# Optimization experiments

Hardware: AMD Instinct MI355X
Metric: run time of the kernel (lower is better)

The kernel has to match this reference:

```python
import jax, jax.numpy as jnp
import numpy as np


def setup_inputs() -> dict:
    key = jax.random.key(0)
    ks = jax.random.split(key, 7)
    B, S, D, H, Dh = 4, 2048, 1024, 16, 64
    return {
        "query_input": jax.random.normal(ks[0], (B, S, D), jnp.float32),
        "key_input": jax.random.normal(ks[1], (B, S, D), jnp.float32),
        "value_input": jax.random.normal(ks[2], (B, S, D), jnp.float32),
        "Wq": jax.random.normal(ks[3], (D, H, Dh), jnp.float32) * 0.03,
        "Wk": jax.random.normal(ks[4], (D, H, Dh), jnp.float32) * 0.03,
        "Wv": jax.random.normal(ks[5], (D, H, Dh), jnp.float32) * 0.03,
        "Wo": jax.random.normal(ks[6], (H, Dh, D), jnp.float32) * 0.03,
    }


def reference(query_input, key_input, value_input, Wq, Wk, Wv, Wo):
    # Projections: [B,S,D] x [D,H,Dh] -> [B,S,H,Dh]
    q = jnp.einsum("bsd,dhk->bshk", query_input, Wq)
    k = jnp.einsum("bsd,dhk->bshk", key_input, Wk)
    v = jnp.einsum("bsd,dhk->bshk", value_input, Wv)
    depth = Wq.shape[-1]
    q = q * (depth ** -0.5)
    # logits: [B,H,F,T]  (F = query len, T = key len)
    logits = jnp.einsum("bthk,bfhk->bhft", k, q)
    weights = jax.nn.softmax(logits, axis=-1)
    # attention output: [B,F,H,Dh]
    ctx = jnp.einsum("bhft,bthk->bfhk", weights, v)
    # output projection: [B,F,H,Dh] x [H,Dh,D] -> [B,F,D]
    return jnp.einsum("bfhk,hkd->bfd", ctx, Wo)
```

## Files before the change

kernel.cpp:

```cpp
#include <hip/hip_runtime.h>
#include <stdint.h>

typedef __bf16 bf16;
typedef __bf16 bf16x4 __attribute__((ext_vector_type(4)));
typedef __bf16 bf16x8 __attribute__((ext_vector_type(8)));
typedef float f32x4 __attribute__((ext_vector_type(4)));

#define AS1 __attribute__((address_space(1)))
#define AS3 __attribute__((address_space(3)))

__device__ __forceinline__ void async16(void* lds, const void* g) {
    __builtin_amdgcn_global_load_lds((AS1 void*)g, (AS3 void*)lds, 16, 0, 0);
}

__global__ __launch_bounds__(256) void prep(
    const float* __restrict__ x0, const float* __restrict__ x1,
    const float* __restrict__ x2,
    bf16* __restrict__ y0, bf16* __restrict__ y1, bf16* __restrict__ y2,
    const float* __restrict__ s0, const float* __restrict__ s1,
    const float* __restrict__ s2, const float* __restrict__ s3,
    bf16* __restrict__ d0, bf16* __restrict__ d1,
    bf16* __restrict__ d2, bf16* __restrict__ d3) {
    const int z = blockIdx.z;
    const int t = threadIdx.x;
    if (z < 3) {
        const float* x = z == 0 ? x0 : z == 1 ? x1 : x2;
        bf16* y = z == 0 ? y0 : z == 1 ? y1 : y2;
        int i = (blockIdx.x * 256 + t) * 8;
        f32x4 a = *(const f32x4*)(x + i);
        f32x4 b = *(const f32x4*)(x + i + 4);
        bf16x8 o;
#pragma unroll
        for (int j = 0; j < 4; ++j) { o[j] = (bf16)a[j]; o[4 + j] = (bf16)b[j]; }
        *(bf16x8*)(y + i) = o;
        return;
    }
    const int bx = blockIdx.x;
    if (bx >= 1024) return;
    const int wsel = bx >> 8, tile = bx & 255;
    const float* W = wsel == 0 ? s0 : wsel == 1 ? s1 : wsel == 2 ? s2 : s3;
    bf16* Wt = wsel == 0 ? d0 : wsel == 1 ? d1 : wsel == 2 ? d2 : d3;
    const int k0 = (tile >> 4) * 64, n0 = (tile & 15) * 64;
    __shared__ float Ts[64 * 65];
    const int c = t & 63, r0 = t >> 6;
#pragma unroll
    for (int i = 0; i < 16; ++i) {
        int r = r0 + i * 4;
        Ts[r * 65 + c] = W[(size_t)(k0 + r) * 1024 + n0 + c];
    }
    __syncthreads();
#pragma unroll
    for (int i = 0; i < 16; ++i) {
        int r = r0 + i * 4;
        Wt[(size_t)(n0 + r) * 1024 + k0 + c] = (bf16)Ts[c * 65 + r];
    }
}

template <typename OutT>
__device__ __forceinline__ void gemm_body(const bf16* __restrict__ A,
                                          const bf16* __restrict__ Bt,
                                          OutT* __restrict__ C,
                                          int N, int K, float scale,
                                          int m0, int n0,
                                          bf16* As, bf16* Bs) {
    const int t = threadIdx.x;
    const int lane = t & 63;
    const int w = t >> 6;
    const int l15 = lane & 15;
    const int quad = lane >> 4;
    const int wm = w >> 1, wn = w & 1;

    f32x4 acc[4][4];
#pragma unroll
    for (int i = 0; i < 4; ++i)
#pragma unroll
        for (int j = 0; j < 4; ++j) acc[i][j] = (f32x4){0.f, 0.f, 0.f, 0.f};

    const bf16* gA[4];
    const bf16* gB[4];
#pragma unroll
    for (int j = 0; j < 4; ++j) {
        int c = j * 256 + t;
        int row = c >> 3, g = (c & 7) ^ (row & 7);
        gA[j] = A + (size_t)(m0 + row) * K + g * 8;
        gB[j] = Bt + (size_t)(n0 + row) * K + g * 8;
    }

    for (int k0 = 0; k0 < K; k0 += 64) {
        __syncthreads();
#pragma unroll
        for (int j = 0; j < 4; ++j) {
            async16(As + (j * 256 + w * 64) * 8, gA[j] + k0);
            async16(Bs + (j * 256 + w * 64) * 8, gB[j] + k0);
        }
        __syncthreads();
#pragma unroll
        for (int kk = 0; kk < 2; ++kk) {
            bf16x8 af[4], bfv[4];
#pragma unroll
            for (int mi = 0; mi < 4; ++mi) {
                int r = wm * 64 + mi * 16 + l15;
                af[mi] = *(const bf16x8*)&As[r * 64 + (((kk * 4 + quad) ^ (r & 7)) * 8)];
            }
#pragma unroll
            for (int ni = 0; ni < 4; ++ni) {
                int r = wn * 64 + ni * 16 + l15;
                bfv[ni] = *(const bf16x8*)&Bs[r * 64 + (((kk * 4 + quad) ^ (r & 7)) * 8)];
            }
#pragma unroll
            for (int mi = 0; mi < 4; ++mi)
#pragma unroll
                for (int ni = 0; ni < 4; ++ni)
                    acc[mi][ni] = __builtin_amdgcn_mfma_f32_16x16x32_bf16(
                        af[mi], bfv[ni], acc[mi][ni], 0, 0, 0);
        }
    }

#pragma unroll
    for (int mi = 0; mi < 4; ++mi)
#pragma unroll
        for (int ni = 0; ni < 4; ++ni)
#pragma unroll
            for (int r = 0; r < 4; ++r) {
                int row = m0 + wm * 64 + mi * 16 + quad * 4 + r;
                int col = n0 + wn * 64 + ni * 16 + l15;
                C[(size_t)row * N + col] = (OutT)(acc[mi][ni][r] * scale);
            }
}

__global__ __launch_bounds__(256) void gemm_qkv(
    const bf16* __restrict__ Xq, const bf16* __restrict__ Xk, const bf16* __restrict__ Xv,
    const bf16* __restrict__ Wqt, const bf16* __restrict__ Wkt, const bf16* __restrict__ Wvt,
    bf16* __restrict__ Qb, bf16* __restrict__ Kb, bf16* __restrict__ VtG) {
    __shared__ __align__(16) bf16 As[128 * 64];
    __shared__ __align__(16) bf16 Bs[128 * 64];
    const int z = blockIdx.z;
    const int blk = blockIdx.x;
    const bf16* A; const bf16* Bt; bf16* C; int N; float scale; int m0, n0;
    if (z == 0) { A = Xq; Bt = Wqt; C = Qb; N = 1024; scale = 0.125f;
                  m0 = (blk >> 3) * 128; n0 = (blk & 7) * 128; }
    else if (z == 1) { A = Xk; Bt = Wkt; C = Kb; N = 1024; scale = 1.0f;
                  m0 = (blk >> 3) * 128; n0 = (blk & 7) * 128; }
    else { A = Wvt; Bt = Xv; C = VtG; N = 8192; scale = 1.0f;
                  m0 = (blk >> 6) * 128; n0 = (blk & 63) * 128; }
    gemm_body<bf16>(A, Bt, C, N, 1024, scale, m0, n0, As, Bs);
}

__global__ __launch_bounds__(256) void gemm_out(const bf16* __restrict__ A,
                                                const bf16* __restrict__ Bt,
                                                float* __restrict__ C) {
    __shared__ __align__(16) bf16 As[128 * 64];
    __shared__ __align__(16) bf16 Bs[128 * 64];
    gemm_body<float>(A, Bt, C, 1024, 1024, 1.0f, blockIdx.y * 128, blockIdx.x * 128,
                     As, Bs);
}

__global__ __launch_bounds__(256) void attn_fa(const bf16* __restrict__ Q,
                                               const bf16* __restrict__ K,
                                               const bf16* __restrict__ Vt,
                                               bf16* __restrict__ O) {
    __shared__ __align__(16) bf16 Ks[2][64 * 64];
    __shared__ __align__(16) bf16 Vs[2][64 * 64];
    __shared__ __align__(16) bf16 Pt[4][32 * 72];

    const int t = threadIdx.x;
    const int lane = t & 63;
    const int w = t >> 6;
    const int l15 = lane & 15;
    const int quad = lane >> 4;
    const int bh = blockIdx.y;
    const int b = bh >> 4, h = bh & 15;
    const int q0 = blockIdx.x * 128;
    const size_t baseQ = (size_t)b * 2048 * 1024 + (size_t)h * 64;
    const float L2E = 1.44269504088896340736f;

    const int r0s = t >> 3,          g0s = (t & 7) ^ (r0s & 7);
    const int r1s = (t + 256) >> 3,  g1s = ((t + 256) & 7) ^ (r1s & 7);
    const bf16* gK0 = K + baseQ + (size_t)r0s * 1024 + g0s * 8;
    const bf16* gK1 = K + baseQ + (size_t)r1s * 1024 + g1s * 8;
    const bf16* gV0 = Vt + (size_t)(h * 64 + r0s) * 8192 + (size_t)b * 2048 + g0s * 8;
    const bf16* gV1 = Vt + (size_t)(h * 64 + r1s) * 8192 + (size_t)b * 2048 + g1s * 8;

    bf16x8 qf[2][2];
#pragma unroll
    for (int mi = 0; mi < 2; ++mi)
#pragma unroll
        for (int kk = 0; kk < 2; ++kk)
            qf[mi][kk] = *(const bf16x8*)(Q + baseQ +
                (size_t)(q0 + w * 32 + mi * 16 + l15) * 1024 + kk * 32 + quad * 8);

    f32x4 accO[4][2];
    float l_part[2] = {0.f, 0.f};
#pragma unroll
    for (int nd = 0; nd < 4; ++nd)
#pragma unroll
        for (int mi = 0; mi < 2; ++mi) accO[nd][mi] = (f32x4){0.f, 0.f, 0.f, 0.f};

    auto swz = [&](int r, int g) { return (r * 8 + (g ^ (r & 7))) * 8; };
    auto stage = [&](int t0, int bi) {
        async16((bf16*)Ks[bi] + w * 512,        gK0 + (size_t)t0 * 1024);
        async16((bf16*)Ks[bi] + 2048 + w * 512, gK1 + (size_t)t0 * 1024);
        async16((bf16*)Vs[bi] + w * 512,        gV0 + t0);
        async16((bf16*)Vs[bi] + 2048 + w * 512, gV1 + t0);
    };

    stage(0, 0);

    for (int it = 0; it < 32; ++it) {
        __syncthreads();
        if (it + 1 < 32) stage((it + 1) * 64, (it + 1) & 1);
        const bf16* Kb = Ks[it & 1];
        const bf16* Vb = Vs[it & 1];

        f32x4 accS[4][2];
#pragma unroll
        for (int nt = 0; nt < 4; ++nt)
#pragma unroll
            for (int mi = 0; mi < 2; ++mi) accS[nt][mi] = (f32x4){0.f, 0.f, 0.f, 0.f};
#pragma unroll
        for (int kk = 0; kk < 2; ++kk) {
            bf16x8 kf[4];
#pragma unroll
            for (int nt = 0; nt < 4; ++nt)
                kf[nt] = *(const bf16x8*)&Kb[swz(nt * 16 + l15, kk * 4 + quad)];
#pragma unroll
            for (int nt = 0; nt < 4; ++nt)
#pragma unroll
                for (int mi = 0; mi < 2; ++mi)
                    accS[nt][mi] = __builtin_amdgcn_mfma_f32_16x16x32_bf16(
                        kf[nt], qf[mi][kk], accS[nt][mi], 0, 0, 0);
        }

        bf16* Pp = &Pt[w][0];
#pragma unroll
        for (int mi = 0; mi < 2; ++mi) {
            float rs = 0.f;
#pragma unroll
            for (int nt = 0; nt < 4; ++nt) {
                bf16x4 pk;
#pragma unroll
                for (int r = 0; r < 4; ++r) {
                    float p = __builtin_amdgcn_exp2f(accS[nt][mi][r] * L2E);
                    rs += p;
                    pk[r] = (bf16)p;
                }
                *(bf16x4*)&Pp[(mi * 16 + l15) * 72 + nt * 16 + quad * 4] = pk;
            }
            l_part[mi] += rs;
        }

#pragma unroll
        for (int kk = 0; kk < 2; ++kk) {
            bf16x8 vf[4], pf[2];
#pragma unroll
            for (int nd = 0; nd < 4; ++nd)
                vf[nd] = *(const bf16x8*)&Vb[swz(nd * 16 + l15, kk * 4 + quad)];
#pragma unroll
            for (int mi = 0; mi < 2; ++mi)
                pf[mi] = *(const bf16x8*)&Pp[(mi * 16 + l15) * 72 + kk * 32 + quad * 8];
#pragma unroll
            for (int nd = 0; nd < 4; ++nd)
#pragma unroll
                for (int mi = 0; mi < 2; ++mi)
                    accO[nd][mi] = __builtin_amdgcn_mfma_f32_16x16x32_bf16(
                        vf[nd], pf[mi], accO[nd][mi], 0, 0, 0);
        }
    }

    float inv[2];
#pragma unroll
    for (int mi = 0; mi < 2; ++mi) {
        float l = l_part[mi];
        l += __shfl_xor(l, 16);
        l += __shfl_xor(l, 32);
        inv[mi] = 1.0f / l;
    }

#pragma unroll
    for (int mi = 0; mi < 2; ++mi) {
        size_t rowoff = baseQ + (size_t)(q0 + w * 32 + mi * 16 + l15) * 1024;
#pragma unroll
        for (int nd = 0; nd < 4; ++nd) {
            bf16x4 o;
#pragma unroll
            for (int r = 0; r < 4; ++r) o[r] = (bf16)(accO[nd][mi][r] * inv[mi]);
            *(bf16x4*)&O[rowoff + nd * 16 + quad * 4] = o;
        }
    }
}

extern "C" void kernel_launch(void* const* d_in, const int* in_sizes, int n_in,
                              void* d_out, int out_size, void* d_ws, size_t ws_size,
                              hipStream_t stream) {
    const float* qin = (const float*)d_in[0];
    const float* kin = (const float*)d_in[1];
    const float* vin = (const float*)d_in[2];
    const float* Wq = (const float*)d_in[3];
    const float* Wk = (const float*)d_in[4];
    const float* Wv = (const float*)d_in[5];
    const float* Wo = (const float*)d_in[6];
    float* out = (float*)d_out;

    char* ws = (char*)d_ws;
    bf16* Xq  = (bf16*)(ws);
    bf16* Xk  = (bf16*)(ws + ((size_t)16 << 20));
    bf16* Xv  = (bf16*)(ws + ((size_t)32 << 20));
    bf16* Qb  = (bf16*)(ws + ((size_t)48 << 20));
    bf16* Kb  = (bf16*)(ws + ((size_t)64 << 20));
    bf16* VtG = (bf16*)(ws + ((size_t)80 << 20));
    bf16* Cb  = (bf16*)(ws);
    bf16* Wqt = (bf16*)(ws + ((size_t)96 << 20));
    bf16* Wkt = Wqt + 1024 * 1024;
    bf16* Wvt = Wkt + 1024 * 1024;
    bf16* Wot = Wvt + 1024 * 1024;

    prep<<<dim3(4096, 1, 4), 256, 0, stream>>>(qin, kin, vin, Xq, Xk, Xv,
                                               Wq, Wk, Wv, Wo, Wqt, Wkt, Wvt, Wot);
    gemm_qkv<<<dim3(512, 1, 3), 256, 0, stream>>>(Xq, Xk, Xv, Wqt, Wkt, Wvt,
                                                  Qb, Kb, VtG);
    attn_fa<<<dim3(16, 64), 256, 0, stream>>>(Qb, Kb, VtG, Cb);
    gemm_out<<<dim3(8, 64), 256, 0, stream>>>(Cb, Wot, out);
}
```

Before: 341.8 us.

## Fold log2e into Q scale, single-buffer K/V, vectorize row-sum accumulation

Folds the log2(e) factor into the Q projection scale so the attention kernel no longer multiplies every logit before exp2. It drops the double-buffered K/V staging in favour of a single buffer, loaded synchronously with a barrier before and after each tile, which halves K/V LDS use and may allow more resident blocks. Row sums now accumulate as 4-wide vectors and are reduced once at the end. The cost is losing the overlap of global loads with compute, so each iteration waits for its K/V tile to arrive.

```diff
diff --git a/kernel.cpp b/kernel.cpp
--- a/kernel.cpp
+++ b/kernel.cpp
@@ -137,7 +137,8 @@
     const int z = blockIdx.z;
     const int blk = blockIdx.x;
     const bf16* A; const bf16* Bt; bf16* C; int N; float scale; int m0, n0;
-    if (z == 0) { A = Xq; Bt = Wqt; C = Qb; N = 1024; scale = 0.125f;
+    if (z == 0) { A = Xq; Bt = Wqt; C = Qb; N = 1024;
+                  scale = 0.125f * 1.44269504088896340736f;
                   m0 = (blk >> 3) * 128; n0 = (blk & 7) * 128; }
     else if (z == 1) { A = Xk; Bt = Wkt; C = Kb; N = 1024; scale = 1.0f;
                   m0 = (blk >> 3) * 128; n0 = (blk & 7) * 128; }
@@ -159,8 +160,8 @@
                                                const bf16* __restrict__ K,
                                                const bf16* __restrict__ Vt,
                                                bf16* __restrict__ O) {
-    __shared__ __align__(16) bf16 Ks[2][64 * 64];
-    __shared__ __align__(16) bf16 Vs[2][64 * 64];
+    __shared__ __align__(16) bf16 Ks[64 * 64];
+    __shared__ __align__(16) bf16 Vs[64 * 64];
     __shared__ __align__(16) bf16 Pt[4][32 * 72];
 
     const int t = threadIdx.x;
@@ -172,7 +173,6 @@
     const int b = bh >> 4, h = bh & 15;
     const int q0 = blockIdx.x * 128;
     const size_t baseQ = (size_t)b * 2048 * 1024 + (size_t)h * 64;
-    const float L2E = 1.44269504088896340736f;
 
     const int r0s = t >> 3,          g0s = (t & 7) ^ (r0s & 7);
     const int r1s = (t + 256) >> 3,  g1s = ((t + 256) & 7) ^ (r1s & 7);
@@ -180,6 +180,10 @@
     const bf16* gK1 = K + baseQ + (size_t)r1s * 1024 + g1s * 8;
     const bf16* gV0 = Vt + (size_t)(h * 64 + r0s) * 8192 + (size_t)b * 2048 + g0s * 8;
     const bf16* gV1 = Vt + (size_t)(h * 64 + r1s) * 8192 + (size_t)b * 2048 + g1s * 8;
+    bf16* lcK0 = (bf16*)Ks + w * 512;
+    bf16* lcK1 = (bf16*)Ks + 2048 + w * 512;
+    bf16* lcV0 = (bf16*)Vs + w * 512;
+    bf16* lcV1 = (bf16*)Vs + 2048 + w * 512;
 
     bf16x8 qf[2][2];
 #pragma unroll
@@ -190,63 +194,63 @@
                 (size_t)(q0 + w * 32 + mi * 16 + l15) * 1024 + kk * 32 + quad * 8);
 
     f32x4 accO[4][2];
-    float l_part[2] = {0.f, 0.f};
+    f32x4 l4[2];
 #pragma unroll
     for (int nd = 0; nd < 4; ++nd)
 #pragma unroll
         for (int mi = 0; mi < 2; ++mi) accO[nd][mi] = (f32x4){0.f, 0.f, 0.f, 0.f};
+    l4[0] = (f32x4){0.f, 0.f, 0.f, 0.f};
+    l4[1] = (f32x4){0.f, 0.f, 0.f, 0.f};
+    const f32x4 z4 = {0.f, 0.f, 0.f, 0.f};
 
     auto swz = [&](int r, int g) { return (r * 8 + (g ^ (r & 7))) * 8; };
-    auto stage = [&](int t0, int bi) {
-        async16((bf16*)Ks[bi] + w * 512,        gK0 + (size_t)t0 * 1024);
-        async16((bf16*)Ks[bi] + 2048 + w * 512, gK1 + (size_t)t0 * 1024);
-        async16((bf16*)Vs[bi] + w * 512,        gV0 + t0);
-        async16((bf16*)Vs[bi] + 2048 + w * 512, gV1 + t0);
-    };
-
-    stage(0, 0);
-
-    for (int it = 0; it < 32; ++it) {
+
+    for (int t0 = 0; t0 < 2048; t0 += 64) {
         __syncthreads();
-        if (it + 1 < 32) stage((it + 1) * 64, (it + 1) & 1);
-        const bf16* Kb = Ks[it & 1];
-        const bf16* Vb = Vs[it & 1];
+        async16(lcK0, gK0 + (size_t)t0 * 1024);
+        async16(lcK1, gK1 + (size_t)t0 * 1024);
+        async16(lcV0, gV0 + t0);
+        async16(lcV1, gV1 + t0);
+        __syncthreads();
 
         f32x4 accS[4][2];
-#pragma unroll
-        for (int nt = 0; nt < 4; ++nt)
-#pragma unroll
-            for (int mi = 0; mi < 2; ++mi) accS[nt][mi] = (f32x4){0.f, 0.f, 0.f, 0.f};
-#pragma unroll
-        for (int kk = 0; kk < 2; ++kk) {
+        {
             bf16x8 kf[4];
 #pragma unroll
             for (int nt = 0; nt < 4; ++nt)
-                kf[nt] = *(const bf16x8*)&Kb[swz(nt * 16 + l15, kk * 4 + quad)];
+                kf[nt] = *(const bf16x8*)&Ks[swz(nt * 16 + l15, quad)];
 #pragma unroll
             for (int nt = 0; nt < 4; ++nt)
 #pragma unroll
                 for (int mi = 0; mi < 2; ++mi)
                     accS[nt][mi] = __builtin_amdgcn_mfma_f32_16x16x32_bf16(
-                        kf[nt], qf[mi][kk], accS[nt][mi], 0, 0, 0);
+                        kf[nt], qf[mi][0], z4, 0, 0, 0);
+#pragma unroll
+            for (int nt = 0; nt < 4; ++nt)
+                kf[nt] = *(const bf16x8*)&Ks[swz(nt * 16 + l15, 4 + quad)];
+#pragma unroll
+            for (int nt = 0; nt < 4; ++nt)
+#pragma unroll
+                for (int mi = 0; mi < 2; ++mi)
+                    accS[nt][mi] = __builtin_amdgcn_mfma_f32_16x16x32_bf16(
+                        kf[nt], qf[mi][1], accS[nt][mi], 0, 0, 0);
         }
 
         bf16* Pp = &Pt[w][0];
 #pragma unroll
         for (int mi = 0; mi < 2; ++mi) {
-            float rs = 0.f;
 #pragma unroll
             for (int nt = 0; nt < 4; ++nt) {
                 bf16x4 pk;
 #pragma unroll
                 for (int r = 0; r < 4; ++r) {
-                    float p = __builtin_amdgcn_exp2f(accS[nt][mi][r] * L2E);
-                    rs += p;
+                    float p = __builtin_amdgcn_exp2f(accS[nt][mi][r]);
+                    accS[nt][mi][r] = p;
                     pk[r] = (bf16)p;
                 }
+                l4[mi] += accS[nt][mi];
                 *(bf16x4*)&Pp[(mi * 16 + l15) * 72 + nt * 16 + quad * 4] = pk;
             }
-            l_part[mi] += rs;
         }
 
 #pragma unroll
@@ -254,7 +258,7 @@
             bf16x8 vf[4], pf[2];
 #pragma unroll
             for (int nd = 0; nd < 4; ++nd)
-                vf[nd] = *(const bf16x8*)&Vb[swz(nd * 16 + l15, kk * 4 + quad)];
+                vf[nd] = *(const bf16x8*)&Vs[swz(nd * 16 + l15, kk * 4 + quad)];
 #pragma unroll
             for (int mi = 0; mi < 2; ++mi)
                 pf[mi] = *(const bf16x8*)&Pp[(mi * 16 + l15) * 72 + kk * 32 + quad * 8];
@@ -270,7 +274,7 @@
     float inv[2];
 #pragma unroll
     for (int mi = 0; mi < 2; ++mi) {
-        float l = l_part[mi];
+        float l = (l4[mi][0] + l4[mi][1]) + (l4[mi][2] + l4[mi][3]);
         l += __shfl_xor(l, 16);
         l += __shfl_xor(l, 32);
         inv[mi] = 1.0f / l;
```

Result: no change. 346.4 us (+1.4%).
